# Optimization experiments

Measured on AMD Instinct MI355X. Metric: run time of the kernel, lower is better.

## Reference

```python
import jax, jax.numpy as jnp
import numpy as np

IN_F = 1024
OUT_F = 512
BATCH = 256
NO_EDGE_OFFSET_T_NORM = 2.0    # identity element offset for min over [0,1] inputs
NO_EDGE_OFFSET_T_CONORM = -1.0 # identity element offset for max over [0,1] inputs


def setup_inputs() -> dict:
    key = jax.random.key(0)
    k1, k2 = jax.random.split(key)
    # fuzzy truth-value inputs in [0, 1]
    x = jax.random.uniform(k1, (BATCH, IN_F), dtype=jnp.float32)
    # logits for gumbel-softmax edge-type selection (module inits to ones)
    edge_type_count = jnp.ones((OUT_F, IN_F, 2), dtype=jnp.float32)
    # uniform noise used to build gumbel noise deterministically
    uniform_noise = jax.random.uniform(k2, (OUT_F, IN_F, 2), dtype=jnp.float32)
    return {"x": x, "edge_type_count": edge_type_count, "uniform_noise": uniform_noise}


def reference(x, edge_type_count, uniform_noise):
    eps = 1e-10
    # hard gumbel-softmax -> only the argmax index is consumed downstream
    gumbel = -jnp.log(-jnp.log(uniform_noise + eps) + eps)
    idx = jnp.argmax(edge_type_count + gumbel, axis=-1)   # [OUT_F, IN_F]; 0 = edge, 1 = no_edge
    is_no_edge = idx == 1                                  # [OUT_F, IN_F]

    # operators cycle [T_Norm.min, T_Conorm.max] across output nodes
    tnorm = (jnp.arange(OUT_F) % 2) == 0                   # [OUT_F]
    offset = jnp.where(tnorm, NO_EDGE_OFFSET_T_NORM, NO_EDGE_OFFSET_T_CONORM).astype(x.dtype)

    # edge value: x for a real edge, 0 + per-operator no_edge offset otherwise
    vals = jnp.where(is_no_edge[None, :, :], offset[None, :, None], x[:, None, :])  # [B, OUT_F, IN_F]

    # per-node t-norm (min) or t-conorm (max) reduction over in_features
    out = jnp.where(tnorm[None, :], jnp.min(vals, axis=-1), jnp.max(vals, axis=-1))  # [B, OUT_F]
    return out
```

## Files before the change

kernel.cpp:

```cpp
#include <hip/hip_runtime.h>
#include <stdint.h>

#define IN_F   1024
#define OUT_F  512
#define BATCH  256

__device__ __forceinline__ float csel(unsigned long long m, float xv, float sent) {
    float r;
    asm("v_cndmask_b32 %0, %1, %2, %3" : "=v"(r) : "v"(sent), "v"(xv), "s"(m));
    return r;
}
__device__ __forceinline__ float vmin3(float a, float b, float c) {
    float r;
    asm("v_min3_f32 %0, %1, %2, %3" : "=v"(r) : "v"(a), "v"(b), "v"(c));
    return r;
}
__device__ __forceinline__ float vmax3(float a, float b, float c) {
    float r;
    asm("v_max3_f32 %0, %1, %2, %3" : "=v"(r) : "v"(a), "v"(b), "v"(c));
    return r;
}
__device__ __forceinline__ unsigned long long uniform_u64(unsigned long long m) {
    unsigned int lo = __builtin_amdgcn_readfirstlane((unsigned int)m);
    unsigned int hi = __builtin_amdgcn_readfirstlane((unsigned int)(m >> 32));
    return ((unsigned long long)hi << 32) | lo;
}

__global__ __launch_bounds__(512, 2) void fused_kernel(
    const float* __restrict__ x,
    const float* __restrict__ etc,
    const float* __restrict__ un,
    float* __restrict__ out)
{
    __shared__ unsigned long long lmask[64];

    int oq   = __builtin_amdgcn_readfirstlane(blockIdx.x >> 1);
    int bh   = __builtin_amdgcn_readfirstlane(blockIdx.x & 1);
    int wv   = threadIdx.x >> 6;
    int lane = threadIdx.x & 63;

    #pragma unroll
    for (int k = 0; k < 8; ++k) {
        int W = wv * 8 + k;
        int s = W >> 4;
        int c = (W >> 2) & 3;
        int j = W & 3;
        int o = oq * 4 + s;
        int i = c * 256 + lane * 4 + j;
        int p = o * IN_F + i;

        float2 e = ((const float2*)etc)[p];
        float2 u = ((const float2*)un)[p];

        float s0 = u.x + 1e-10f;
        float l0 = (float)log((double)s0);
        float m0 = -l0 + 1e-10f;
        float g0 = -(float)log((double)m0);
        float t0 = e.x + g0;

        float s1 = u.y + 1e-10f;
        float l1 = (float)log((double)s1);
        float m1 = -l1 + 1e-10f;
        float g1 = -(float)log((double)m1);
        float t1 = e.y + g1;

        unsigned long long bits = __ballot(!(t1 > t0));
        if (lane == 0) lmask[W] = bits;
    }
    __syncthreads();

    const float4* xq = (const float4*)x;
    bool hi = (lane & 32) != 0;
    int obase = oq * 4;

    for (int tile = 0; tile < 2; ++tile) {
        int bp0 = (bh << 6) + (wv << 3) + (tile << 2);

        float acc[4][4][2];
        #pragma unroll
        for (int q = 0; q < 4; ++q)
            #pragma unroll
            for (int s = 0; s < 4; ++s) {
                float S = (s & 1) ? -1.0f : 2.0f;
                acc[q][s][0] = S;
                acc[q][s][1] = S;
            }

        #pragma unroll
        for (int c = 0; c < 4; ++c) {
            unsigned long long mk[16];
            #pragma unroll
            for (int s = 0; s < 4; ++s)
                #pragma unroll
                for (int j = 0; j < 4; ++j)
                    mk[s * 4 + j] = uniform_u64(lmask[s * 16 + c * 4 + j]);

            #pragma unroll
            for (int q = 0; q < 4; ++q) {
                int b0 = (bp0 + q) << 1;
                float4 va = xq[(b0 + 0) * (IN_F / 4) + c * 64 + lane];
                float4 vb = xq[(b0 + 1) * (IN_F / 4) + c * 64 + lane];
                #pragma unroll
                for (int s = 0; s < 4; ++s) {
                    float S = (s & 1) ? -1.0f : 2.0f;
                    float e0a = csel(mk[s*4+0], va.x, S);
                    float e1a = csel(mk[s*4+1], va.y, S);
                    float e2a = csel(mk[s*4+2], va.z, S);
                    float e3a = csel(mk[s*4+3], va.w, S);
                    float e0b = csel(mk[s*4+0], vb.x, S);
                    float e1b = csel(mk[s*4+1], vb.y, S);
                    float e2b = csel(mk[s*4+2], vb.z, S);
                    float e3b = csel(mk[s*4+3], vb.w, S);
                    if (s & 1) {
                        acc[q][s][0] = vmax3(acc[q][s][0], vmax3(e0a, e1a, e2a), e3a);
                        acc[q][s][1] = vmax3(acc[q][s][1], vmax3(e0b, e1b, e2b), e3b);
                    } else {
                        acc[q][s][0] = vmin3(acc[q][s][0], vmin3(e0a, e1a, e2a), e3a);
                        acc[q][s][1] = vmin3(acc[q][s][1], vmin3(e0b, e1b, e2b), e3b);
                    }
                }
            }
        }

        #pragma unroll
        for (int q = 0; q < 4; ++q) {
            int b0 = (bp0 + q) << 1;
            float z[4];
            #pragma unroll
            for (int s = 0; s < 4; ++s) {
                float aA = acc[q][s][0], aB = acc[q][s][1];
                float cr = hi ? aA : aB;
                float pp = __shfl_xor(cr, 32, 64);
                float zz = hi ? aB : aA;
                if (s & 1) {
                    zz = fmaxf(zz, pp);
                    #pragma unroll
                    for (int d = 16; d; d >>= 1) zz = fmaxf(zz, __shfl_xor(zz, d, 64));
                } else {
                    zz = fminf(zz, pp);
                    #pragma unroll
                    for (int d = 16; d; d >>= 1) zz = fminf(zz, __shfl_xor(zz, d, 64));
                }
                z[s] = zz;
            }
            if ((lane & 31) == 0) {
                int b = b0 + (lane >> 5);
                float4 o4 = make_float4(z[0], z[1], z[2], z[3]);
                *((float4*)(out + b * OUT_F + obase)) = o4;
            }
        }
    }
}

extern "C" void kernel_launch(void* const* d_in, const int* in_sizes, int n_in,
                              void* d_out, int out_size, void* d_ws, size_t ws_size,
                              hipStream_t stream) {
    const float* x   = (const float*)d_in[0];
    const float* etc = (const float*)d_in[1];
    const float* un  = (const float*)d_in[2];
    float* out = (float*)d_out;
    (void)d_ws; (void)ws_size;

    hipLaunchKernelGGL(fused_kernel, dim3(256), dim3(512), 0, stream,
                       x, etc, un, out);
}
```

Baseline: 87.21 us.

## Split fused kernel into mask-generation and reduction kernels via workspace

The single fused kernel becomes two kernels. The first computes the Gumbel argmax bitmasks over the edge logits and noise across 2048 blocks and writes them to a global workspace. The second reads those masks from global memory as uniform scalar loads, with each wave handling 8 output nodes for 2 batch rows over 2048 blocks. The aim is more parallelism for the expensive double-precision log work and better occupancy in the reduction. In exchange it adds a second launch and a round trip of the masks through global memory, and x is reread by many more waves.

```diff
diff --git a/kernel.cpp b/kernel.cpp
--- a/kernel.cpp
+++ b/kernel.cpp
@@ -4,6 +4,37 @@
 #define IN_F   1024
 #define OUT_F  512
 #define BATCH  256
+
+__global__ __launch_bounds__(256) void mask_kernel(
+    const float* __restrict__ etc,
+    const float* __restrict__ un,
+    unsigned long long* __restrict__ mask_t)
+{
+    int o = blockIdx.x >> 2;
+    int c = blockIdx.x & 3;
+    int j = threadIdx.x >> 6;
+    int l = threadIdx.x & 63;
+    int i = c * 256 + l * 4 + j;
+    int p = o * IN_F + i;
+
+    float2 e = ((const float2*)etc)[p];
+    float2 u = ((const float2*)un)[p];
+
+    float s0 = u.x + 1e-10f;
+    float l0 = (float)log((double)s0);
+    float m0 = -l0 + 1e-10f;
+    float g0 = -(float)log((double)m0);
+    float t0 = e.x + g0;
+
+    float s1 = u.y + 1e-10f;
+    float l1 = (float)log((double)s1);
+    float m1 = -l1 + 1e-10f;
+    float g1 = -(float)log((double)m1);
+    float t1 = e.y + g1;
+
+    unsigned long long bits = __ballot(!(t1 > t0));
+    if (l == 0) mask_t[o * 16 + c * 4 + j] = bits;
+}
 
 __device__ __forceinline__ float csel(unsigned long long m, float xv, float sent) {
     float r;
@@ -20,135 +51,86 @@
     asm("v_max3_f32 %0, %1, %2, %3" : "=v"(r) : "v"(a), "v"(b), "v"(c));
     return r;
 }
-__device__ __forceinline__ unsigned long long uniform_u64(unsigned long long m) {
-    unsigned int lo = __builtin_amdgcn_readfirstlane((unsigned int)m);
-    unsigned int hi = __builtin_amdgcn_readfirstlane((unsigned int)(m >> 32));
-    return ((unsigned long long)hi << 32) | lo;
-}
 
-__global__ __launch_bounds__(512, 2) void fused_kernel(
+__global__ __launch_bounds__(256, 8) void reduce_kernel(
     const float* __restrict__ x,
-    const float* __restrict__ etc,
-    const float* __restrict__ un,
+    const unsigned long long* __restrict__ mask_t,
     float* __restrict__ out)
 {
-    __shared__ unsigned long long lmask[64];
+    int wave = threadIdx.x >> 6;
+    int lane = threadIdx.x & 63;
+    int T  = blockIdx.x * 4 + wave;
+    int bp = __builtin_amdgcn_readfirstlane(T >> 6);
+    int og = __builtin_amdgcn_readfirstlane(T & 63);
 
-    int oq   = __builtin_amdgcn_readfirstlane(blockIdx.x >> 1);
-    int bh   = __builtin_amdgcn_readfirstlane(blockIdx.x & 1);
-    int wv   = threadIdx.x >> 6;
-    int lane = threadIdx.x & 63;
+    const float4* xA = (const float4*)(x + (bp * 2 + 0) * IN_F);
+    const float4* xB = (const float4*)(x + (bp * 2 + 1) * IN_F);
+
+    int ob = og * 8;
+    const unsigned long long* mw = mask_t + ob * 16;
+
+    bool hi = (lane & 32) != 0;
+
+    float accA[8], accB[8];
+    #pragma unroll
+    for (int s = 0; s < 8; ++s) {
+        float S = (s & 1) ? -1.0f : 2.0f;
+        accA[s] = S;
+        accB[s] = S;
+    }
 
     #pragma unroll
-    for (int k = 0; k < 8; ++k) {
-        int W = wv * 8 + k;
-        int s = W >> 4;
-        int c = (W >> 2) & 3;
-        int j = W & 3;
-        int o = oq * 4 + s;
-        int i = c * 256 + lane * 4 + j;
-        int p = o * IN_F + i;
-
-        float2 e = ((const float2*)etc)[p];
-        float2 u = ((const float2*)un)[p];
-
-        float s0 = u.x + 1e-10f;
-        float l0 = (float)log((double)s0);
-        float m0 = -l0 + 1e-10f;
-        float g0 = -(float)log((double)m0);
-        float t0 = e.x + g0;
-
-        float s1 = u.y + 1e-10f;
-        float l1 = (float)log((double)s1);
-        float m1 = -l1 + 1e-10f;
-        float g1 = -(float)log((double)m1);
-        float t1 = e.y + g1;
-
-        unsigned long long bits = __ballot(!(t1 > t0));
-        if (lane == 0) lmask[W] = bits;
-    }
-    __syncthreads();
-
-    const float4* xq = (const float4*)x;
-    bool hi = (lane & 32) != 0;
-    int obase = oq * 4;
-
-    for (int tile = 0; tile < 2; ++tile) {
-        int bp0 = (bh << 6) + (wv << 3) + (tile << 2);
-
-        float acc[4][4][2];
+    for (int c = 0; c < 4; ++c) {
+        float4 va = xA[c * 64 + lane];
+        float4 vb = xB[c * 64 + lane];
         #pragma unroll
-        for (int q = 0; q < 4; ++q)
-            #pragma unroll
-            for (int s = 0; s < 4; ++s) {
-                float S = (s & 1) ? -1.0f : 2.0f;
-                acc[q][s][0] = S;
-                acc[q][s][1] = S;
-            }
-
-        #pragma unroll
-        for (int c = 0; c < 4; ++c) {
-            unsigned long long mk[16];
-            #pragma unroll
-            for (int s = 0; s < 4; ++s)
-                #pragma unroll
-                for (int j = 0; j < 4; ++j)
-                    mk[s * 4 + j] = uniform_u64(lmask[s * 16 + c * 4 + j]);
-
-            #pragma unroll
-            for (int q = 0; q < 4; ++q) {
-                int b0 = (bp0 + q) << 1;
-                float4 va = xq[(b0 + 0) * (IN_F / 4) + c * 64 + lane];
-                float4 vb = xq[(b0 + 1) * (IN_F / 4) + c * 64 + lane];
-                #pragma unroll
-                for (int s = 0; s < 4; ++s) {
-                    float S = (s & 1) ? -1.0f : 2.0f;
-                    float e0a = csel(mk[s*4+0], va.x, S);
-                    float e1a = csel(mk[s*4+1], va.y, S);
-                    float e2a = csel(mk[s*4+2], va.z, S);
-                    float e3a = csel(mk[s*4+3], va.w, S);
-                    float e0b = csel(mk[s*4+0], vb.x, S);
-                    float e1b = csel(mk[s*4+1], vb.y, S);
-                    float e2b = csel(mk[s*4+2], vb.z, S);
-                    float e3b = csel(mk[s*4+3], vb.w, S);
-                    if (s & 1) {
-                        acc[q][s][0] = vmax3(acc[q][s][0], vmax3(e0a, e1a, e2a), e3a);
-                        acc[q][s][1] = vmax3(acc[q][s][1], vmax3(e0b, e1b, e2b), e3b);
-                    } else {
-                        acc[q][s][0] = vmin3(acc[q][s][0], vmin3(e0a, e1a, e2a), e3a);
-                        acc[q][s][1] = vmin3(acc[q][s][1], vmin3(e0b, e1b, e2b), e3b);
-                    }
-                }
+        for (int s = 0; s < 8; ++s) {
+            unsigned long long m0 = mw[s * 16 + c * 4 + 0];
+            unsigned long long m1 = mw[s * 16 + c * 4 + 1];
+            unsigned long long m2 = mw[s * 16 + c * 4 + 2];
+            unsigned long long m3 = mw[s * 16 + c * 4 + 3];
+            float S = (s & 1) ? -1.0f : 2.0f;
+            float e0a = csel(m0, va.x, S);
+            float e1a = csel(m1, va.y, S);
+            float e2a = csel(m2, va.z, S);
+            float e3a = csel(m3, va.w, S);
+            float e0b = csel(m0, vb.x, S);
+            float e1b = csel(m1, vb.y, S);
+            float e2b = csel(m2, vb.z, S);
+            float e3b = csel(m3, vb.w, S);
+            if (s & 1) {
+                accA[s] = vmax3(accA[s], vmax3(e0a, e1a, e2a), e3a);
+                accB[s] = vmax3(accB[s], vmax3(e0b, e1b, e2b), e3b);
+            } else {
+                accA[s] = vmin3(accA[s], vmin3(e0a, e1a, e2a), e3a);
+                accB[s] = vmin3(accB[s], vmin3(e0b, e1b, e2b), e3b);
             }
         }
+    }
 
-        #pragma unroll
-        for (int q = 0; q < 4; ++q) {
-            int b0 = (bp0 + q) << 1;
-            float z[4];
+    float z[8];
+    #pragma unroll
+    for (int s = 0; s < 8; ++s) {
+        float cr = hi ? accA[s] : accB[s];
+        float pp = __shfl_xor(cr, 32, 64);
+        float zz = hi ? accB[s] : accA[s];
+        if (s & 1) {
+            zz = fmaxf(zz, pp);
             #pragma unroll
-            for (int s = 0; s < 4; ++s) {
-                float aA = acc[q][s][0], aB = acc[q][s][1];
-                float cr = hi ? aA : aB;
-                float pp = __shfl_xor(cr, 32, 64);
-                float zz = hi ? aB : aA;
-                if (s & 1) {
-                    zz = fmaxf(zz, pp);
-                    #pragma unroll
-                    for (int d = 16; d; d >>= 1) zz = fmaxf(zz, __shfl_xor(zz, d, 64));
-                } else {
-                    zz = fminf(zz, pp);
-                    #pragma unroll
-                    for (int d = 16; d; d >>= 1) zz = fminf(zz, __shfl_xor(zz, d, 64));
-                }
-                z[s] = zz;
-            }
-            if ((lane & 31) == 0) {
-                int b = b0 + (lane >> 5);
-                float4 o4 = make_float4(z[0], z[1], z[2], z[3]);
-                *((float4*)(out + b * OUT_F + obase)) = o4;
-            }
+            for (int d = 16; d; d >>= 1) zz = fmaxf(zz, __shfl_xor(zz, d, 64));
+        } else {
+            zz = fminf(zz, pp);
+            #pragma unroll
+            for (int d = 16; d; d >>= 1) zz = fminf(zz, __shfl_xor(zz, d, 64));
         }
+        z[s] = zz;
+    }
+
+    if ((lane & 31) == 0) {
+        int b = bp * 2 + (lane >> 5);
+        float* ob_ptr = out + b * OUT_F + ob;
+        *((float4*)(ob_ptr + 0)) = make_float4(z[0], z[1], z[2], z[3]);
+        *((float4*)(ob_ptr + 4)) = make_float4(z[4], z[5], z[6], z[7]);
     }
 }
 
@@ -159,8 +141,10 @@
     const float* etc = (const float*)d_in[1];
     const float* un  = (const float*)d_in[2];
     float* out = (float*)d_out;
-    (void)d_ws; (void)ws_size;
+    unsigned long long* mask_t = (unsigned long long*)d_ws;
 
-    hipLaunchKernelGGL(fused_kernel, dim3(256), dim3(512), 0, stream,
-                       x, etc, un, out);
+    hipLaunchKernelGGL(mask_kernel, dim3(OUT_F * 4), dim3(256), 0, stream,
+                       etc, un, mask_t);
+    hipLaunchKernelGGL(reduce_kernel, dim3(BATCH * OUT_F / 16 / 4), dim3(256), 0, stream,
+                       x, mask_t, out);
 }
```

Measured after the change: 77.33 us. -11.3%, faster.
